# Kernel optimization log

Hardware: AMD Instinct MI355X
Metric: run time of the kernel (lower is better)

Reference implementation:

```python
import jax, jax.numpy as jnp
import numpy as np

GAMMA = 2.0  # args.gamma
B, C, H, W = 8, 21, 512, 512


def setup_inputs() -> dict:
    key = jax.random.key(0)
    k1, k2 = jax.random.split(key)
    pred = jax.random.normal(k1, (B, C, H, W), dtype=jnp.float32)
    # one-hot target built from random per-pixel class labels
    labels = jax.random.randint(k2, (B, H, W), 0, C)
    target = jax.nn.one_hot(labels, C, dtype=jnp.float32)  # [B,H,W,C]
    target = jnp.transpose(target, (0, 3, 1, 2))  # [B,C,H,W]
    return {"pred": pred, "target": target}


def reference(pred, target) -> jnp.ndarray:
    b, c, h, w = pred.shape
    logits = jax.nn.log_softmax(pred, axis=1)  # [B,C,H,W]
    lo = jnp.transpose(logits, (0, 2, 3, 1)).reshape(-1, c)  # [N,C]
    tg = jnp.transpose(target, (0, 2, 3, 1)).reshape(-1, c)  # [N,C]
    n = lo.shape[0]
    beta = (n - 1.0) / n
    # per-pixel focal term summed over channels: sum_j (1-p_j)^gamma * log p_j * t_j
    row_val = jnp.sum((1.0 - jnp.exp(lo)) ** GAMMA * lo * tg, axis=1)  # [N]
    mask = (tg == 1).astype(lo.dtype)  # [N,C] class membership mask
    n_c = jnp.sum(mask, axis=0)  # [C] pixels per class
    class_sum = jnp.einsum('nc,n->c', mask, row_val)  # [C] masked reductions
    w = (1.0 - beta) / (1.0 - jnp.power(jnp.float32(beta), n_c) + 1e-6)  # [C]
    return -jnp.sum(w * class_sum) / n
```

## Files before the change

kernel.cpp:

```cpp
#include <hip/hip_runtime.h>

#define BBATCH 8
#define CCH    21
#define HWSZ   (512*512)
#define NPIX   (BBATCH*HWSZ)
#define BLKT   256

__global__ __launch_bounds__(BLKT) void cb_focal_partial(
    const float* __restrict__ pred, const float* __restrict__ targ,
    float* __restrict__ psum, unsigned* __restrict__ pcnt)
{
    __shared__ float    ls_sum[CCH];
    __shared__ unsigned ls_cnt[CCH];
    if (threadIdx.x < CCH) { ls_sum[threadIdx.x] = 0.f; ls_cnt[threadIdx.x] = 0u; }
    __syncthreads();

    const int stride = gridDim.x * blockDim.x;
    for (int p = blockIdx.x * blockDim.x + threadIdx.x; p < NPIX; p += stride) {
        const int b  = p >> 18;
        const int hw = p & (HWSZ - 1);
        const float* pp = pred + (size_t)b * (CCH * HWSZ) + hw;
        const float* tp = targ + (size_t)b * (CCH * HWSZ) + hw;

        float v[CCH];
        float m = -1e30f, vy = 0.f;
        int   y = 0;
        #pragma unroll
        for (int c = 0; c < CCH; ++c) {
            const float val = pp[(size_t)c * HWSZ];
            const float t   = tp[(size_t)c * HWSZ];
            v[c] = val;
            m = fmaxf(m, val);
            const bool hit = t > 0.5f;
            y  = hit ? c   : y;
            vy = hit ? val : vy;
        }
        float s = 0.f;
        #pragma unroll
        for (int c = 0; c < CCH; ++c) s += __expf(v[c] - m);

        const float logp = vy - m - __logf(s);
        const float pe   = __expf(logp);
        const float om   = 1.f - pe;
        const float rv   = om * om * logp;

        atomicAdd(&ls_sum[y], rv);
        atomicAdd(&ls_cnt[y], 1u);
    }
    __syncthreads();
    if (threadIdx.x < CCH) {
        psum[(size_t)threadIdx.x * gridDim.x + blockIdx.x] = ls_sum[threadIdx.x];
        pcnt[(size_t)threadIdx.x * gridDim.x + blockIdx.x] = ls_cnt[threadIdx.x];
    }
}

__global__ __launch_bounds__(1024) void cb_focal_final(
    const float* __restrict__ psum, const unsigned* __restrict__ pcnt,
    float* __restrict__ out, int nblk)
{
    __shared__ double s_cls[CCH];
    __shared__ double s_cnt[CCH];
    const int wave = threadIdx.x >> 6;
    const int lane = threadIdx.x & 63;

    for (int c = wave; c < CCH; c += 16) {
        double   s   = 0.0;
        unsigned cnt = 0u;
        for (int i = lane; i < nblk; i += 64) {
            s   += (double)psum[(size_t)c * nblk + i];
            cnt += pcnt[(size_t)c * nblk + i];
        }
        for (int off = 32; off; off >>= 1) {
            s   += __shfl_down(s, off, 64);
            cnt += __shfl_down(cnt, off, 64);
        }
        if (lane == 0) { s_cls[c] = s; s_cnt[c] = (double)cnt; }
    }
    __syncthreads();

    if (threadIdx.x == 0) {
        const double n    = (double)NPIX;
        const double beta = (n - 1.0) / n;
        double loss = 0.0;
        for (int c = 0; c < CCH; ++c) {
            const double w = (1.0 - beta) / (1.0 - pow(beta, s_cnt[c]) + 1e-6);
            loss += w * s_cls[c];
        }
        out[0] = (float)(-loss / n);
    }
}

extern "C" void kernel_launch(void* const* d_in, const int* in_sizes, int n_in,
                              void* d_out, int out_size, void* d_ws, size_t ws_size,
                              hipStream_t stream) {
    const float* pred = (const float*)d_in[0];
    const float* targ = (const float*)d_in[1];
    float* out = (float*)d_out;

    int nblk = 2048;
    const size_t per_blk = (size_t)CCH * (sizeof(float) + sizeof(unsigned));
    if (ws_size < (size_t)nblk * per_blk) {
        nblk = (int)(ws_size / per_blk);
        if (nblk < 1) nblk = 1;
    }
    float*    psum = (float*)d_ws;
    unsigned* pcnt = (unsigned*)((char*)d_ws + (size_t)CCH * nblk * sizeof(float));

    cb_focal_partial<<<nblk, BLKT, 0, stream>>>(pred, targ, psum, pcnt);
    cb_focal_final<<<1, 1024, 0, stream>>>(psum, pcnt, out, nblk);
}
```

Before: 408.5 us.

## Vectorize loads to float4, drop max-subtraction, use global atomics for class sums

Each thread now handles four adjacent pixels through float4 loads of pred and target, and the kernel is launched with one thread per four pixels instead of a grid-stride loop. The softmax no longer subtracts the max, so the exp is computed once per element and reused for the target probability. Per-block partials go to 21 global float atomics, replacing the workspace partial arrays and the larger final reduction. This needs an extra zeroing kernel, makes the float reduction order nondeterministic, risks overflow on large logits, and counts pixels in float, which loses exactness above about 16.7M per class.

```diff
diff --git a/kernel.cpp b/kernel.cpp
--- a/kernel.cpp
+++ b/kernel.cpp
@@ -3,109 +3,93 @@
 #define BBATCH 8
 #define CCH    21
 #define HWSZ   (512*512)
+#define HW4    (HWSZ/4)
 #define NPIX   (BBATCH*HWSZ)
 #define BLKT   256
+#define NBLK   (NPIX/4/BLKT)
+
+__global__ void cb_zero(float* __restrict__ acc) {
+    if (threadIdx.x < 2 * CCH) acc[threadIdx.x] = 0.f;
+}
 
 __global__ __launch_bounds__(BLKT) void cb_focal_partial(
-    const float* __restrict__ pred, const float* __restrict__ targ,
-    float* __restrict__ psum, unsigned* __restrict__ pcnt)
+    const float4* __restrict__ pred4, const float4* __restrict__ targ4,
+    float* __restrict__ gsum, float* __restrict__ gcnt)
 {
-    __shared__ float    ls_sum[CCH];
-    __shared__ unsigned ls_cnt[CCH];
-    if (threadIdx.x < CCH) { ls_sum[threadIdx.x] = 0.f; ls_cnt[threadIdx.x] = 0u; }
+    __shared__ float ls_sum[CCH];
+    __shared__ float ls_cnt[CCH];
+    if (threadIdx.x < CCH) { ls_sum[threadIdx.x] = 0.f; ls_cnt[threadIdx.x] = 0.f; }
     __syncthreads();
 
-    const int stride = gridDim.x * blockDim.x;
-    for (int p = blockIdx.x * blockDim.x + threadIdx.x; p < NPIX; p += stride) {
-        const int b  = p >> 18;
-        const int hw = p & (HWSZ - 1);
-        const float* pp = pred + (size_t)b * (CCH * HWSZ) + hw;
-        const float* tp = targ + (size_t)b * (CCH * HWSZ) + hw;
+    const int tid = blockIdx.x * BLKT + threadIdx.x;
+    const int b   = tid >> 16;
+    const int hw4 = tid & (HW4 - 1);
+    const float4* pp = pred4 + (size_t)b * CCH * HW4 + hw4;
+    const float4* tp = targ4 + (size_t)b * CCH * HW4 + hw4;
 
-        float v[CCH];
-        float m = -1e30f, vy = 0.f;
-        int   y = 0;
-        #pragma unroll
-        for (int c = 0; c < CCH; ++c) {
-            const float val = pp[(size_t)c * HWSZ];
-            const float t   = tp[(size_t)c * HWSZ];
-            v[c] = val;
-            m = fmaxf(m, val);
-            const bool hit = t > 0.5f;
-            y  = hit ? c   : y;
-            vy = hit ? val : vy;
-        }
-        float s = 0.f;
-        #pragma unroll
-        for (int c = 0; c < CCH; ++c) s += __expf(v[c] - m);
+    float s0 = 0.f, s1 = 0.f, s2 = 0.f, s3 = 0.f;
+    float vy0 = 0.f, vy1 = 0.f, vy2 = 0.f, vy3 = 0.f;
+    float ey0 = 1.f, ey1 = 1.f, ey2 = 1.f, ey3 = 1.f;
+    int   y0 = 0, y1 = 0, y2 = 0, y3 = 0;
 
-        const float logp = vy - m - __logf(s);
-        const float pe   = __expf(logp);
-        const float om   = 1.f - pe;
-        const float rv   = om * om * logp;
+    #pragma unroll
+    for (int c = 0; c < CCH; ++c) {
+        const float4 v = pp[(size_t)c * HW4];
+        const float4 t = tp[(size_t)c * HW4];
+        const float e0 = __expf(v.x), e1 = __expf(v.y),
+                    e2 = __expf(v.z), e3 = __expf(v.w);
+        s0 += e0; s1 += e1; s2 += e2; s3 += e3;
+        const bool h0 = t.x > 0.5f, h1 = t.y > 0.5f,
+                   h2 = t.z > 0.5f, h3 = t.w > 0.5f;
+        y0 = h0 ? c : y0;  vy0 = h0 ? v.x : vy0;  ey0 = h0 ? e0 : ey0;
+        y1 = h1 ? c : y1;  vy1 = h1 ? v.y : vy1;  ey1 = h1 ? e1 : ey1;
+        y2 = h2 ? c : y2;  vy2 = h2 ? v.z : vy2;  ey2 = h2 ? e2 : ey2;
+        y3 = h3 ? c : y3;  vy3 = h3 ? v.w : vy3;  ey3 = h3 ? e3 : ey3;
+    }
 
-        atomicAdd(&ls_sum[y], rv);
-        atomicAdd(&ls_cnt[y], 1u);
+    {
+        const float l0 = vy0 - __logf(s0), p0 = ey0 / s0, o0 = 1.f - p0;
+        const float l1 = vy1 - __logf(s1), p1 = ey1 / s1, o1 = 1.f - p1;
+        const float l2 = vy2 - __logf(s2), p2 = ey2 / s2, o2 = 1.f - p2;
+        const float l3 = vy3 - __logf(s3), p3 = ey3 / s3, o3 = 1.f - p3;
+        atomicAdd(&ls_sum[y0], o0 * o0 * l0);  atomicAdd(&ls_cnt[y0], 1.f);
+        atomicAdd(&ls_sum[y1], o1 * o1 * l1);  atomicAdd(&ls_cnt[y1], 1.f);
+        atomicAdd(&ls_sum[y2], o2 * o2 * l2);  atomicAdd(&ls_cnt[y2], 1.f);
+        atomicAdd(&ls_sum[y3], o3 * o3 * l3);  atomicAdd(&ls_cnt[y3], 1.f);
     }
     __syncthreads();
     if (threadIdx.x < CCH) {
-        psum[(size_t)threadIdx.x * gridDim.x + blockIdx.x] = ls_sum[threadIdx.x];
-        pcnt[(size_t)threadIdx.x * gridDim.x + blockIdx.x] = ls_cnt[threadIdx.x];
+        atomicAdd(&gsum[threadIdx.x], ls_sum[threadIdx.x]);
+        atomicAdd(&gcnt[threadIdx.x], ls_cnt[threadIdx.x]);
     }
 }
 
-__global__ __launch_bounds__(1024) void cb_focal_final(
-    const float* __restrict__ psum, const unsigned* __restrict__ pcnt,
-    float* __restrict__ out, int nblk)
+__global__ void cb_focal_final(const float* __restrict__ gsum,
+                               const float* __restrict__ gcnt,
+                               float* __restrict__ out)
 {
-    __shared__ double s_cls[CCH];
-    __shared__ double s_cnt[CCH];
-    const int wave = threadIdx.x >> 6;
-    const int lane = threadIdx.x & 63;
-
-    for (int c = wave; c < CCH; c += 16) {
-        double   s   = 0.0;
-        unsigned cnt = 0u;
-        for (int i = lane; i < nblk; i += 64) {
-            s   += (double)psum[(size_t)c * nblk + i];
-            cnt += pcnt[(size_t)c * nblk + i];
-        }
-        for (int off = 32; off; off >>= 1) {
-            s   += __shfl_down(s, off, 64);
-            cnt += __shfl_down(cnt, off, 64);
-        }
-        if (lane == 0) { s_cls[c] = s; s_cnt[c] = (double)cnt; }
-    }
-    __syncthreads();
-
-    if (threadIdx.x == 0) {
+    const int lane = threadIdx.x;
+    double term = 0.0;
+    if (lane < CCH) {
         const double n    = (double)NPIX;
         const double beta = (n - 1.0) / n;
-        double loss = 0.0;
-        for (int c = 0; c < CCH; ++c) {
-            const double w = (1.0 - beta) / (1.0 - pow(beta, s_cnt[c]) + 1e-6);
-            loss += w * s_cls[c];
-        }
-        out[0] = (float)(-loss / n);
+        const double w = (1.0 - beta) / (1.0 - pow(beta, (double)gcnt[lane]) + 1e-6);
+        term = w * (double)gsum[lane];
     }
+    for (int off = 32; off; off >>= 1) term += __shfl_down(term, off, 64);
+    if (lane == 0) out[0] = (float)(-term / (double)NPIX);
 }
 
 extern "C" void kernel_launch(void* const* d_in, const int* in_sizes, int n_in,
                               void* d_out, int out_size, void* d_ws, size_t ws_size,
                               hipStream_t stream) {
-    const float* pred = (const float*)d_in[0];
-    const float* targ = (const float*)d_in[1];
-    float* out = (float*)d_out;
+    const float4* pred4 = (const float4*)d_in[0];
+    const float4* targ4 = (const float4*)d_in[1];
+    float* out  = (float*)d_out;
+    float* gsum = (float*)d_ws;
+    float* gcnt = gsum + CCH;
 
-    int nblk = 2048;
-    const size_t per_blk = (size_t)CCH * (sizeof(float) + sizeof(unsigned));
-    if (ws_size < (size_t)nblk * per_blk) {
-        nblk = (int)(ws_size / per_blk);
-        if (nblk < 1) nblk = 1;
-    }
-    float*    psum = (float*)d_ws;
-    unsigned* pcnt = (unsigned*)((char*)d_ws + (size_t)CCH * nblk * sizeof(float));
-
-    cb_focal_partial<<<nblk, BLKT, 0, stream>>>(pred, targ, psum, pcnt);
-    cb_focal_final<<<1, 1024, 0, stream>>>(psum, pcnt, out, nblk);
+    cb_zero<<<1, 64, 0, stream>>>(gsum);
+    cb_focal_partial<<<NBLK, BLKT, 0, stream>>>(pred4, targ4, gsum, gcnt);
+    cb_focal_final<<<1, 64, 0, stream>>>(gsum, gcnt, out);
 }
```

Result: faster. 359.0 us (-12.1%).
